# Performance work log

Measured on AMD Instinct MI355X. Metric: run time of the kernel, lower is better.

Reference implementation:

```python
import jax, jax.numpy as jnp
import numpy as np

N = 4194304   # variable nodes
M = 2097152   # check nodes
DC = 10       # max check degree


def setup_inputs() -> dict:
    key = jax.random.key(0)
    k1, k2 = jax.random.split(key)
    cn_adj = jax.random.randint(k1, (M, DC), 0, N, dtype=jnp.int32)
    # pad: last neighbor slot of every other check is empty (-1)
    cn_adj = cn_adj.at[:, -1].set(jnp.where(jnp.arange(M) % 2 == 0, -1, cn_adj[:, -1]))
    llr0 = jax.random.normal(k2, (N,), jnp.float32)
    gamma = jnp.ones((), jnp.float32)  # learnable scaling (learn_gamma=True)
    return {"llr0": llr0, "gamma": gamma, "cn_adj": cn_adj, "n_iter": 5}


def _bp(llr0, gamma, cn_adj, n_iter):
    n = llr0.shape[0]
    valid = cn_adj >= 0
    # original gathers v2c[cn_adj] with raw -1 entries -> numpy-style wrap to index n-1
    gather_idx = jnp.where(valid, cn_adj, n - 1)
    # original masks padded slots out of the scatter-add only
    scatter_idx = jnp.where(valid, cn_adj, 0)

    def bp_step(v2c, _):
        msgs = v2c[gather_idx]                               # (M, DC) gather
        sign = jnp.prod(jnp.sign(msgs + 1e-12), axis=1)      # (M,)
        mag = jnp.min(jnp.abs(msgs), axis=1)                 # (M,) min-sum magnitude
        c2v = gamma * sign * mag                             # (M,) scaled min-sum
        msg = jnp.where(valid, c2v[:, None], 0.0)            # mask padded edges
        v_sum = jnp.zeros(n, llr0.dtype).at[scatter_idx].add(msg)  # scatter-add to variables
        return llr0 + v_sum - v2c, None

    v2c0 = jnp.zeros(n, llr0.dtype)
    v2c_final, _ = jax.lax.scan(bp_step, v2c0, None, length=n_iter)
    return llr0 + v2c_final


def reference(llr0, gamma, cn_adj, n_iter):
    return _bp(llr0, gamma, cn_adj, n_iter)
```

## Files before the change

### kernel.cpp

```cpp
#include <hip/hip_runtime.h>
#include <hip/hip_fp16.h>

#define DCC 10
#define NB 2048
#define NBLK 256
#define HTHREADS 1024

typedef int iv4 __attribute__((ext_vector_type(4)));


__global__ __launch_bounds__(256) void bp_init2_kernel(
    const float* __restrict__ llr0, float* __restrict__ v2c,
    unsigned short* __restrict__ v2c_h, int Nq) {
  int i = blockIdx.x * blockDim.x + threadIdx.x;
  if (i >= Nq) return;
  float4 l = reinterpret_cast<const float4*>(llr0)[i];
  reinterpret_cast<float4*>(v2c)[i] = l;
  reinterpret_cast<__half2*>(v2c_h)[2 * i]     = __floats2half2_rn(l.x, l.y);
  reinterpret_cast<__half2*>(v2c_h)[2 * i + 1] = __floats2half2_rn(l.z, l.w);
}

__global__ __launch_bounds__(HTHREADS) void bp_hist_kernel(
    const int* __restrict__ adj, unsigned* __restrict__ hist,
    int i4_per_block, int i4_total) {
  __shared__ unsigned h[NB];
  for (int i = threadIdx.x; i < NB; i += HTHREADS) h[i] = 0u;
  __syncthreads();
  const iv4* p = reinterpret_cast<const iv4*>(adj);
  int base = blockIdx.x * i4_per_block;
  int lim = base + i4_per_block;
  if (lim > i4_total) lim = i4_total;
  for (int g = base + (int)threadIdx.x; g < lim; g += HTHREADS) {
    iv4 r = __builtin_nontemporal_load(p + g);
    if (r.x >= 0) atomicAdd(&h[(unsigned)r.x >> 11], 1u);
    if (r.y >= 0) atomicAdd(&h[(unsigned)r.y >> 11], 1u);
    if (r.z >= 0) atomicAdd(&h[(unsigned)r.z >> 11], 1u);
    if (r.w >= 0) atomicAdd(&h[(unsigned)r.w >> 11], 1u);
  }
  __syncthreads();
  for (int i = threadIdx.x; i < NB; i += HTHREADS)
    hist[(size_t)i * NBLK + blockIdx.x] = h[i];
}

__global__ __launch_bounds__(256) void bp_scan1_kernel(
    unsigned* __restrict__ data, unsigned* __restrict__ sums) {
  __shared__ unsigned ts[256];
  const int base = blockIdx.x * 1024;
  uint4 d = reinterpret_cast<const uint4*>(data + base)[threadIdx.x];
  unsigned tsum = d.x + d.y + d.z + d.w;
  ts[threadIdx.x] = tsum;
  __syncthreads();
  for (int off = 1; off < 256; off <<= 1) {
    unsigned add = ((int)threadIdx.x >= off) ? ts[threadIdx.x - off] : 0u;
    __syncthreads();
    ts[threadIdx.x] += add;
    __syncthreads();
  }
  unsigned run = ts[threadIdx.x] - tsum;
  if (threadIdx.x == 255) sums[blockIdx.x] = ts[255];
  uint4 o;
  o.x = run; run += d.x;
  o.y = run; run += d.y;
  o.z = run; run += d.z;
  o.w = run;
  reinterpret_cast<uint4*>(data + base)[threadIdx.x] = o;
}

__global__ __launch_bounds__(256) void bp_scan2_kernel(
    unsigned* __restrict__ sums, unsigned* __restrict__ total_p, int n) {
  __shared__ unsigned ts[256];
  __shared__ unsigned carry_s;
  if (threadIdx.x == 0) carry_s = 0u;
  __syncthreads();
  for (int c = 0; c < n; c += 256) {
    int idx = c + (int)threadIdx.x;
    unsigned orig = (idx < n) ? sums[idx] : 0u;
    ts[threadIdx.x] = orig;
    __syncthreads();
    for (int off = 1; off < 256; off <<= 1) {
      unsigned add = ((int)threadIdx.x >= off) ? ts[threadIdx.x - off] : 0u;
      __syncthreads();
      ts[threadIdx.x] += add;
      __syncthreads();
    }
    unsigned excl = ts[threadIdx.x] - orig + carry_s;
    if (idx < n) sums[idx] = excl;
    __syncthreads();
    if (threadIdx.x == 0) carry_s += ts[255];
    __syncthreads();
  }
  if (threadIdx.x == 0) *total_p = carry_s;
}

__global__ __launch_bounds__(HTHREADS) void bp_sortscatter_kernel(
    const int* __restrict__ adj, const unsigned* __restrict__ hist_s,
    const unsigned* __restrict__ sums_s, unsigned* __restrict__ recs,
    int i4_per_block, int i4_total) {
  __shared__ unsigned cur[NB];
  for (int i = threadIdx.x; i < NB; i += HTHREADS) {
    unsigned idx = (unsigned)i * NBLK + blockIdx.x;
    cur[i] = hist_s[idx] + sums_s[idx >> 10];
  }
  __syncthreads();
  const iv4* p = reinterpret_cast<const iv4*>(adj);
  int base = blockIdx.x * i4_per_block;
  int lim = base + i4_per_block;
  if (lim > i4_total) lim = i4_total;
  for (int g = base + (int)threadIdx.x; g < lim; g += HTHREADS) {
    iv4 r = __builtin_nontemporal_load(p + g);
    int s4 = g * 4;
    int av[4] = {r.x, r.y, r.z, r.w};
#pragma unroll
    for (int j = 0; j < 4; ++j) {
      int ai = av[j];
      if (ai >= 0) {
        unsigned check = (unsigned)(s4 + j) / DCC;
        unsigned pos = atomicAdd(&cur[(unsigned)ai >> 11], 1u);
        recs[pos] = ((unsigned)(ai & (NB - 1)) << 21) | check;
      }
    }
  }
}

__global__ __launch_bounds__(256) void bp_gather1_kernel(
    const int* __restrict__ adj, const unsigned short* __restrict__ v2c_h,
    unsigned* __restrict__ state, int Mhalf, int N, int lo, int hi) {
  int t = blockIdx.x * blockDim.x + threadIdx.x;
  if (t >= Mhalf) return;
  const iv4* p = reinterpret_cast<const iv4*>(adj + (size_t)t * 2 * DCC);
  iv4 r0 = __builtin_nontemporal_load(p);
  iv4 r1 = __builtin_nontemporal_load(p + 1);
  iv4 r2 = __builtin_nontemporal_load(p + 2);
  iv4 r3 = __builtin_nontemporal_load(p + 3);
  iv4 r4 = __builtin_nontemporal_load(p + 4);
  int a[20] = {r0.x, r0.y, r0.z, r0.w, r1.x, r1.y, r1.z, r1.w,
               r2.x, r2.y, r2.z, r2.w, r3.x, r3.y, r3.z, r3.w,
               r4.x, r4.y, r4.z, r4.w};
  unsigned s2[2];
#pragma unroll
  for (int c = 0; c < 2; ++c) {
    unsigned sgn = 0u;
    unsigned mab = 0x7c00u;
#pragma unroll
    for (int j = 0; j < DCC; ++j) {
      int ai = a[c * DCC + j];
      int gi = (ai >= 0) ? ai : (N - 1);
      if (gi >= lo && gi < hi) {
        unsigned hb = (unsigned)v2c_h[gi];
        unsigned ab = hb & 0x7fffu;
        sgn ^= (ab != 0u) ? (hb & 0x8000u) : 0u;
        mab = (ab < mab) ? ab : mab;
      }
    }
    s2[c] = mab | sgn;
  }
  state[t] = s2[0] | (s2[1] << 16);
}

__global__ __launch_bounds__(256) void bp_gather2_kernel(
    const int* __restrict__ adj, const unsigned short* __restrict__ v2c_h,
    const unsigned* __restrict__ state0, unsigned short* __restrict__ c2v_h,
    const float* __restrict__ gamma_p, int Mhalf, int N, int lo, int hi) {
  int t = blockIdx.x * blockDim.x + threadIdx.x;
  if (t >= Mhalf) return;
  const float gamma = *gamma_p;
  const iv4* p = reinterpret_cast<const iv4*>(adj + (size_t)t * 2 * DCC);
  iv4 r0 = __builtin_nontemporal_load(p);
  iv4 r1 = __builtin_nontemporal_load(p + 1);
  iv4 r2 = __builtin_nontemporal_load(p + 2);
  iv4 r3 = __builtin_nontemporal_load(p + 3);
  iv4 r4 = __builtin_nontemporal_load(p + 4);
  int a[20] = {r0.x, r0.y, r0.z, r0.w, r1.x, r1.y, r1.z, r1.w,
               r2.x, r2.y, r2.z, r2.w, r3.x, r3.y, r3.z, r3.w,
               r4.x, r4.y, r4.z, r4.w};
  unsigned p0 = state0[t];
  unsigned outw = 0u;
#pragma unroll
  for (int c = 0; c < 2; ++c) {
    unsigned sgn = 0u;
    unsigned mab = 0x7c00u;
#pragma unroll
    for (int j = 0; j < DCC; ++j) {
      int ai = a[c * DCC + j];
      int gi = (ai >= 0) ? ai : (N - 1);
      if (gi >= lo && gi < hi) {
        unsigned hb = (unsigned)v2c_h[gi];
        unsigned ab = hb & 0x7fffu;
        sgn ^= (ab != 0u) ? (hb & 0x8000u) : 0u;
        mab = (ab < mab) ? ab : mab;
      }
    }
    unsigned q0 = (c == 0) ? (p0 & 0xffffu) : (p0 >> 16);
    unsigned a0 = q0 & 0x7fffu;
    unsigned ab = (a0 < mab) ? a0 : mab;
    unsigned sg = ((q0 ^ sgn) & 0x8000u);
    float val = gamma * __half2float(__ushort_as_half((unsigned short)ab));
    val = __uint_as_float(__float_as_uint(val) ^ (sg << 16));
    outw |= ((unsigned)__half_as_ushort(__float2half_rn(val))) << (16 * c);
  }
  reinterpret_cast<unsigned*>(c2v_h)[t] = outw;
}

__global__ __launch_bounds__(256) void bp_accvar_kernel(
    const unsigned* __restrict__ recs, const unsigned short* __restrict__ c2v_h,
    const unsigned* __restrict__ hist_s, const unsigned* __restrict__ sums_s,
    const unsigned* __restrict__ total_p, const float* __restrict__ llr0,
    float* __restrict__ v2c, unsigned short* __restrict__ v2c_h,
    float* __restrict__ out) {
  __shared__ __align__(16) float acc[NB];
  const int b = blockIdx.x;
  for (int i = threadIdx.x; i < NB; i += 256) acc[i] = 0.0f;
  unsigned i0 = (unsigned)b * NBLK;
  unsigned start = hist_s[i0] + sums_s[i0 >> 10];
  unsigned end = (b == NB - 1)
                     ? *total_p
                     : (hist_s[i0 + NBLK] + sums_s[(i0 + NBLK) >> 10]);
  __syncthreads();
  for (unsigned e = start + threadIdx.x; e < end; e += 256) {
    unsigned rec = recs[e];
    float val = __half2float(__ushort_as_half(c2v_h[rec & 0x1FFFFFu]));
    atomicAdd(&acc[rec >> 21], val);
  }
  __syncthreads();
  const int gq = b * (NB / 4);
#pragma unroll
  for (int k = 0; k < 2; ++k) {
    int li = k * 256 + (int)threadIdx.x;
    int gi = gq + li;
    float4 l = reinterpret_cast<const float4*>(llr0)[gi];
    float4 v = reinterpret_cast<float4*>(v2c)[gi];
    float4 s = reinterpret_cast<const float4*>(acc)[li];
    float4 nv;
    nv.x = l.x + s.x - v.x;
    nv.y = l.y + s.y - v.y;
    nv.z = l.z + s.z - v.z;
    nv.w = l.w + s.w - v.w;
    reinterpret_cast<float4*>(v2c)[gi] = nv;
    reinterpret_cast<__half2*>(v2c_h)[2 * gi]     = __floats2half2_rn(nv.x, nv.y);
    reinterpret_cast<__half2*>(v2c_h)[2 * gi + 1] = __floats2half2_rn(nv.z, nv.w);
    if (out != nullptr) {
      float4 o;
      o.x = l.x + nv.x;
      o.y = l.y + nv.y;
      o.z = l.z + nv.z;
      o.w = l.w + nv.w;
      reinterpret_cast<float4*>(out)[gi] = o;
    }
  }
}


__global__ __launch_bounds__(256) void bp_init_kernel(
    const float* __restrict__ llr0, float* __restrict__ v2c,
    float* __restrict__ vsum, __half* __restrict__ v2c_h, int Nq) {
  int i = blockIdx.x * blockDim.x + threadIdx.x;
  if (i >= Nq) return;
  float4 l = reinterpret_cast<const float4*>(llr0)[i];
  reinterpret_cast<float4*>(v2c)[i] = l;
  reinterpret_cast<float4*>(vsum)[i] = make_float4(0.f, 0.f, 0.f, 0.f);
  reinterpret_cast<__half2*>(v2c_h)[2 * i]     = __floats2half2_rn(l.x, l.y);
  reinterpret_cast<__half2*>(v2c_h)[2 * i + 1] = __floats2half2_rn(l.z, l.w);
}

__global__ __launch_bounds__(256) void bp_check_kernel(
    const int* __restrict__ adj, const __half* __restrict__ v2c_h,
    float* __restrict__ vsum, const float* __restrict__ gamma_p,
    int Mhalf, int N) {
  int t = blockIdx.x * blockDim.x + threadIdx.x;
  if (t >= Mhalf) return;
  const float gamma = *gamma_p;
  const int4* p = reinterpret_cast<const int4*>(adj + (size_t)t * 2 * DCC);
  int4 r0 = p[0], r1 = p[1], r2 = p[2], r3 = p[3], r4 = p[4];
  int a[20] = {r0.x, r0.y, r0.z, r0.w, r1.x, r1.y, r1.z, r1.w,
               r2.x, r2.y, r2.z, r2.w, r3.x, r3.y, r3.z, r3.w,
               r4.x, r4.y, r4.z, r4.w};
#pragma unroll
  for (int c = 0; c < 2; ++c) {
    unsigned sgnbits = 0u;
    float mag = 3.402823466e+38f;
#pragma unroll
    for (int j = 0; j < DCC; ++j) {
      int ai = a[c * DCC + j];
      int gi = (ai >= 0) ? ai : (N - 1);
      float v = __half2float(v2c_h[gi]);
      sgnbits ^= (__float_as_uint(v + 1e-12f) & 0x80000000u);
      mag = fminf(mag, fabsf(v));
    }
    float c2v = __uint_as_float(__float_as_uint(gamma * mag) ^ sgnbits);
#pragma unroll
    for (int j = 0; j < DCC; ++j) {
      int ai = a[c * DCC + j];
      if (ai >= 0) unsafeAtomicAdd(&vsum[ai], c2v);
    }
  }
}

__global__ __launch_bounds__(256) void bp_var_kernel(
    const float* __restrict__ llr0, float* __restrict__ v2c,
    float* __restrict__ vsum, __half* __restrict__ v2c_h,
    float* __restrict__ out, int Nq) {
  int i = blockIdx.x * blockDim.x + threadIdx.x;
  if (i >= Nq) return;
  float4 l = reinterpret_cast<const float4*>(llr0)[i];
  float4 v = reinterpret_cast<float4*>(v2c)[i];
  float4 s = reinterpret_cast<float4*>(vsum)[i];
  float4 nv;
  nv.x = l.x + s.x - v.x;
  nv.y = l.y + s.y - v.y;
  nv.z = l.z + s.z - v.z;
  nv.w = l.w + s.w - v.w;
  reinterpret_cast<float4*>(v2c)[i] = nv;
  reinterpret_cast<float4*>(vsum)[i] = make_float4(0.f, 0.f, 0.f, 0.f);
  reinterpret_cast<__half2*>(v2c_h)[2 * i]     = __floats2half2_rn(nv.x, nv.y);
  reinterpret_cast<__half2*>(v2c_h)[2 * i + 1] = __floats2half2_rn(nv.z, nv.w);
  if (out != nullptr) {
    float4 o;
    o.x = l.x + nv.x;
    o.y = l.y + nv.y;
    o.z = l.z + nv.z;
    o.w = l.w + nv.w;
    reinterpret_cast<float4*>(out)[i] = o;
  }
}


extern "C" void kernel_launch(void* const* d_in, const int* in_sizes, int n_in,
                              void* d_out, int out_size, void* d_ws, size_t ws_size,
                              hipStream_t stream) {
  const float* llr0  = (const float*)d_in[0];
  const float* gamma = (const float*)d_in[1];
  const int*   adj   = (const int*)d_in[2];
  const int N = in_sizes[0];
  const int M = in_sizes[2] / DCC;
  const int Mh = M / 2;
  const int NITER = 5;
  const int Nq = N / 4;
  const int varBlocks = (Nq + 255) / 256;
  const int chkBlocks = (Mh + 255) / 256;
  const int Nh = N / 2;

  char* w = (char*)d_ws;
  auto carve = [&](size_t bytes) {
    char* r = w;
    w += (bytes + 255) & ~(size_t)255;
    return r;
  };
  float*          v2c    = (float*)carve((size_t)N * 4);
  unsigned short* v2c_h  = (unsigned short*)carve((size_t)N * 2);
  unsigned*       state0 = (unsigned*)carve((size_t)Mh * 4);
  unsigned short* c2v_h  = (unsigned short*)carve((size_t)M * 2);
  unsigned*       hist   = (unsigned*)carve((size_t)NB * NBLK * 4);
  unsigned*       sums   = (unsigned*)carve((size_t)513 * 4);
  unsigned*       recs   = (unsigned*)carve((size_t)M * DCC * 4);
  unsigned*       total_p = sums + 512;
  size_t need = (size_t)(w - (char*)d_ws);

  const int i4_total = (M * DCC) / 4;
  const int i4_per_block = (i4_total + NBLK - 1) / NBLK;

  bool fast = (need <= ws_size) && (N == NB * 2048) && (M <= (1 << 21)) &&
              ((M * DCC) % 4 == 0);

  if (fast) {
    bp_init2_kernel<<<varBlocks, 256, 0, stream>>>(llr0, v2c, v2c_h, Nq);
    bp_hist_kernel<<<NBLK, HTHREADS, 0, stream>>>(adj, hist, i4_per_block, i4_total);
    bp_scan1_kernel<<<(NB * NBLK) / 1024, 256, 0, stream>>>(hist, sums);
    bp_scan2_kernel<<<1, 256, 0, stream>>>(sums, total_p, (NB * NBLK) / 1024);
    bp_sortscatter_kernel<<<NBLK, HTHREADS, 0, stream>>>(adj, hist, sums, recs,
                                                         i4_per_block, i4_total);
    for (int it = 1; it < NITER; ++it) {
      bp_gather1_kernel<<<chkBlocks, 256, 0, stream>>>(
          adj, v2c_h, state0, Mh, N, 0, Nh);
      bp_gather2_kernel<<<chkBlocks, 256, 0, stream>>>(
          adj, v2c_h, state0, c2v_h, gamma, Mh, N, Nh, N);
      float* outp = (it == NITER - 1) ? (float*)d_out : nullptr;
      bp_accvar_kernel<<<NB, 256, 0, stream>>>(
          recs, c2v_h, hist, sums, total_p, llr0, v2c, v2c_h, outp);
    }
  } else {
    float*  fv2c   = (float*)d_ws;
    float*  fvsum  = fv2c + N;
    __half* fv2c_h = (__half*)(fvsum + N);
    bp_init_kernel<<<varBlocks, 256, 0, stream>>>(llr0, fv2c, fvsum, fv2c_h, Nq);
    for (int it = 1; it < NITER; ++it) {
      bp_check_kernel<<<chkBlocks, 256, 0, stream>>>(adj, fv2c_h, fvsum, gamma, Mh, N);
      float* outp = (it == NITER - 1) ? (float*)d_out : nullptr;
      bp_var_kernel<<<varBlocks, 256, 0, stream>>>(llr0, fv2c, fvsum, fv2c_h, outp, Nq);
    }
  }
}
```

Measured before the change: 1.547 ms.

## Fuse split-range gather kernels into one pass and trim final-iteration stores

Replaces the two gather kernels, which each covered half of the variable index range to keep the fp16 v2c table cache-resident, with a single kernel that gathers all neighbors at once. This drops the intermediate state buffer and the second read of the adjacency array. The final iteration now writes only the output, skipping the v2c and v2c_h updates. The histogram block count is also halved, which changes the sort and scan granularity. The cost is that random gathers now span the full 8 MB half table instead of a 4 MB slice, so more of them may miss in cache.

```diff
diff --git a/kernel.cpp b/kernel.cpp
--- a/kernel.cpp
+++ b/kernel.cpp
@@ -3,7 +3,7 @@
 
 #define DCC 10
 #define NB 2048
-#define NBLK 256
+#define NBLK 128
 #define HTHREADS 1024
 
 typedef int iv4 __attribute__((ext_vector_type(4)));
@@ -122,45 +122,10 @@
   }
 }
 
-__global__ __launch_bounds__(256) void bp_gather1_kernel(
+__global__ __launch_bounds__(256) void bp_gatherf_kernel(
     const int* __restrict__ adj, const unsigned short* __restrict__ v2c_h,
-    unsigned* __restrict__ state, int Mhalf, int N, int lo, int hi) {
-  int t = blockIdx.x * blockDim.x + threadIdx.x;
-  if (t >= Mhalf) return;
-  const iv4* p = reinterpret_cast<const iv4*>(adj + (size_t)t * 2 * DCC);
-  iv4 r0 = __builtin_nontemporal_load(p);
-  iv4 r1 = __builtin_nontemporal_load(p + 1);
-  iv4 r2 = __builtin_nontemporal_load(p + 2);
-  iv4 r3 = __builtin_nontemporal_load(p + 3);
-  iv4 r4 = __builtin_nontemporal_load(p + 4);
-  int a[20] = {r0.x, r0.y, r0.z, r0.w, r1.x, r1.y, r1.z, r1.w,
-               r2.x, r2.y, r2.z, r2.w, r3.x, r3.y, r3.z, r3.w,
-               r4.x, r4.y, r4.z, r4.w};
-  unsigned s2[2];
-#pragma unroll
-  for (int c = 0; c < 2; ++c) {
-    unsigned sgn = 0u;
-    unsigned mab = 0x7c00u;
-#pragma unroll
-    for (int j = 0; j < DCC; ++j) {
-      int ai = a[c * DCC + j];
-      int gi = (ai >= 0) ? ai : (N - 1);
-      if (gi >= lo && gi < hi) {
-        unsigned hb = (unsigned)v2c_h[gi];
-        unsigned ab = hb & 0x7fffu;
-        sgn ^= (ab != 0u) ? (hb & 0x8000u) : 0u;
-        mab = (ab < mab) ? ab : mab;
-      }
-    }
-    s2[c] = mab | sgn;
-  }
-  state[t] = s2[0] | (s2[1] << 16);
-}
-
-__global__ __launch_bounds__(256) void bp_gather2_kernel(
-    const int* __restrict__ adj, const unsigned short* __restrict__ v2c_h,
-    const unsigned* __restrict__ state0, unsigned short* __restrict__ c2v_h,
-    const float* __restrict__ gamma_p, int Mhalf, int N, int lo, int hi) {
+    unsigned short* __restrict__ c2v_h, const float* __restrict__ gamma_p,
+    int Mhalf, int N) {
   int t = blockIdx.x * blockDim.x + threadIdx.x;
   if (t >= Mhalf) return;
   const float gamma = *gamma_p;
@@ -173,7 +138,6 @@
   int a[20] = {r0.x, r0.y, r0.z, r0.w, r1.x, r1.y, r1.z, r1.w,
                r2.x, r2.y, r2.z, r2.w, r3.x, r3.y, r3.z, r3.w,
                r4.x, r4.y, r4.z, r4.w};
-  unsigned p0 = state0[t];
   unsigned outw = 0u;
 #pragma unroll
   for (int c = 0; c < 2; ++c) {
@@ -183,19 +147,13 @@
     for (int j = 0; j < DCC; ++j) {
       int ai = a[c * DCC + j];
       int gi = (ai >= 0) ? ai : (N - 1);
-      if (gi >= lo && gi < hi) {
-        unsigned hb = (unsigned)v2c_h[gi];
-        unsigned ab = hb & 0x7fffu;
-        sgn ^= (ab != 0u) ? (hb & 0x8000u) : 0u;
-        mab = (ab < mab) ? ab : mab;
-      }
-    }
-    unsigned q0 = (c == 0) ? (p0 & 0xffffu) : (p0 >> 16);
-    unsigned a0 = q0 & 0x7fffu;
-    unsigned ab = (a0 < mab) ? a0 : mab;
-    unsigned sg = ((q0 ^ sgn) & 0x8000u);
-    float val = gamma * __half2float(__ushort_as_half((unsigned short)ab));
-    val = __uint_as_float(__float_as_uint(val) ^ (sg << 16));
+      unsigned hb = (unsigned)v2c_h[gi];
+      unsigned ab = hb & 0x7fffu;
+      sgn ^= (ab != 0u) ? (hb & 0x8000u) : 0u;
+      mab = (ab < mab) ? ab : mab;
+    }
+    float val = gamma * __half2float(__ushort_as_half((unsigned short)mab));
+    val = __uint_as_float(__float_as_uint(val) ^ (sgn << 16));
     outw |= ((unsigned)__half_as_ushort(__float2half_rn(val))) << (16 * c);
   }
   reinterpret_cast<unsigned*>(c2v_h)[t] = outw;
@@ -235,9 +193,6 @@
     nv.y = l.y + s.y - v.y;
     nv.z = l.z + s.z - v.z;
     nv.w = l.w + s.w - v.w;
-    reinterpret_cast<float4*>(v2c)[gi] = nv;
-    reinterpret_cast<__half2*>(v2c_h)[2 * gi]     = __floats2half2_rn(nv.x, nv.y);
-    reinterpret_cast<__half2*>(v2c_h)[2 * gi + 1] = __floats2half2_rn(nv.z, nv.w);
     if (out != nullptr) {
       float4 o;
       o.x = l.x + nv.x;
@@ -245,6 +200,10 @@
       o.z = l.z + nv.z;
       o.w = l.w + nv.w;
       reinterpret_cast<float4*>(out)[gi] = o;
+    } else {
+      reinterpret_cast<float4*>(v2c)[gi] = nv;
+      reinterpret_cast<__half2*>(v2c_h)[2 * gi]     = __floats2half2_rn(nv.x, nv.y);
+      reinterpret_cast<__half2*>(v2c_h)[2 * gi + 1] = __floats2half2_rn(nv.z, nv.w);
     }
   }
 }
@@ -337,7 +296,6 @@
   const int Nq = N / 4;
   const int varBlocks = (Nq + 255) / 256;
   const int chkBlocks = (Mh + 255) / 256;
-  const int Nh = N / 2;
 
   char* w = (char*)d_ws;
   auto carve = [&](size_t bytes) {
@@ -347,7 +305,6 @@
   };
   float*          v2c    = (float*)carve((size_t)N * 4);
   unsigned short* v2c_h  = (unsigned short*)carve((size_t)N * 2);
-  unsigned*       state0 = (unsigned*)carve((size_t)Mh * 4);
   unsigned short* c2v_h  = (unsigned short*)carve((size_t)M * 2);
   unsigned*       hist   = (unsigned*)carve((size_t)NB * NBLK * 4);
   unsigned*       sums   = (unsigned*)carve((size_t)513 * 4);
@@ -357,6 +314,7 @@
 
   const int i4_total = (M * DCC) / 4;
   const int i4_per_block = (i4_total + NBLK - 1) / NBLK;
+  const int scanN = (NB * NBLK) / 1024;
 
   bool fast = (need <= ws_size) && (N == NB * 2048) && (M <= (1 << 21)) &&
               ((M * DCC) % 4 == 0);
@@ -364,15 +322,13 @@
   if (fast) {
     bp_init2_kernel<<<varBlocks, 256, 0, stream>>>(llr0, v2c, v2c_h, Nq);
     bp_hist_kernel<<<NBLK, HTHREADS, 0, stream>>>(adj, hist, i4_per_block, i4_total);
-    bp_scan1_kernel<<<(NB * NBLK) / 1024, 256, 0, stream>>>(hist, sums);
-    bp_scan2_kernel<<<1, 256, 0, stream>>>(sums, total_p, (NB * NBLK) / 1024);
+    bp_scan1_kernel<<<scanN, 256, 0, stream>>>(hist, sums);
+    bp_scan2_kernel<<<1, 256, 0, stream>>>(sums, total_p, scanN);
     bp_sortscatter_kernel<<<NBLK, HTHREADS, 0, stream>>>(adj, hist, sums, recs,
                                                          i4_per_block, i4_total);
     for (int it = 1; it < NITER; ++it) {
-      bp_gather1_kernel<<<chkBlocks, 256, 0, stream>>>(
-          adj, v2c_h, state0, Mh, N, 0, Nh);
-      bp_gather2_kernel<<<chkBlocks, 256, 0, stream>>>(
-          adj, v2c_h, state0, c2v_h, gamma, Mh, N, Nh, N);
+      bp_gatherf_kernel<<<chkBlocks, 256, 0, stream>>>(
+          adj, v2c_h, c2v_h, gamma, Mh, N);
       float* outp = (it == NITER - 1) ? (float*)d_out : nullptr;
       bp_accvar_kernel<<<NB, 256, 0, stream>>>(
           recs, c2v_h, hist, sums, total_p, llr0, v2c, v2c_h, outp);
```

Result: slower. 1.793 ms (+15.9%).

## Buffer sort-scatter records in LDS and flush per-bin chunks of eight

Applied to the files above, without the earlier changes.

The counting-sort scatter now stages records per bin in an 8-entry shared-memory ring and flushes each full group of eight as contiguous global writes, instead of issuing one random 4-byte global store per edge. This is meant to improve write coalescing in the one-time edge bucketing pass, at the cost of 80 KB+ of LDS per block, two extra barriers per phase, and lower occupancy. Separately, the last iteration's accumulate kernel skips writing v2c and v2c_h, since only the output is needed after it.

```diff
diff --git a/kernel.cpp b/kernel.cpp
--- a/kernel.cpp
+++ b/kernel.cpp
@@ -96,29 +96,57 @@
     const int* __restrict__ adj, const unsigned* __restrict__ hist_s,
     const unsigned* __restrict__ sums_s, unsigned* __restrict__ recs,
     int i4_per_block, int i4_total) {
-  __shared__ unsigned cur[NB];
+  __shared__ unsigned gstart[NB];
+  __shared__ unsigned cnt[NB];
+  __shared__ unsigned flushed[NB];
+  __shared__ unsigned buf[NB * 8];
   for (int i = threadIdx.x; i < NB; i += HTHREADS) {
     unsigned idx = (unsigned)i * NBLK + blockIdx.x;
-    cur[i] = hist_s[idx] + sums_s[idx >> 10];
+    gstart[i] = hist_s[idx] + sums_s[idx >> 10];
+    cnt[i] = 0u;
+    flushed[i] = 0u;
   }
   __syncthreads();
   const iv4* p = reinterpret_cast<const iv4*>(adj);
   int base = blockIdx.x * i4_per_block;
   int lim = base + i4_per_block;
   if (lim > i4_total) lim = i4_total;
-  for (int g = base + (int)threadIdx.x; g < lim; g += HTHREADS) {
-    iv4 r = __builtin_nontemporal_load(p + g);
-    int s4 = g * 4;
-    int av[4] = {r.x, r.y, r.z, r.w};
-#pragma unroll
-    for (int j = 0; j < 4; ++j) {
-      int ai = av[j];
-      if (ai >= 0) {
-        unsigned check = (unsigned)(s4 + j) / DCC;
-        unsigned pos = atomicAdd(&cur[(unsigned)ai >> 11], 1u);
-        recs[pos] = ((unsigned)(ai & (NB - 1)) << 21) | check;
+  for (int ph = base; ph < lim; ph += HTHREADS) {
+    int g = ph + (int)threadIdx.x;
+    if (g < lim) {
+      iv4 r = __builtin_nontemporal_load(p + g);
+      int s4 = g * 4;
+      int av[4] = {r.x, r.y, r.z, r.w};
+#pragma unroll
+      for (int j = 0; j < 4; ++j) {
+        int ai = av[j];
+        if (ai >= 0) {
+          unsigned bin = (unsigned)ai >> 11;
+          unsigned rec =
+              ((unsigned)(ai & (NB - 1)) << 21) | ((unsigned)(s4 + j) / DCC);
+          unsigned pos = atomicAdd(&cnt[bin], 1u);
+          if (pos < flushed[bin] + 8u)
+            buf[bin * 8 + (pos & 7u)] = rec;
+          else
+            recs[gstart[bin] + pos] = rec;
+        }
       }
     }
+    __syncthreads();
+    for (int b = threadIdx.x; b < NB; b += HTHREADS) {
+      unsigned c = cnt[b], f = flushed[b];
+      if (c - f >= 8u) {
+        unsigned gp = gstart[b] + f;
+#pragma unroll
+        for (int k = 0; k < 8; ++k) recs[gp + k] = buf[b * 8 + ((f + k) & 7u)];
+        flushed[b] = c;
+      }
+    }
+    __syncthreads();
+  }
+  for (int b = threadIdx.x; b < NB; b += HTHREADS) {
+    unsigned c = cnt[b], f = flushed[b], gp = gstart[b];
+    for (unsigned q = f; q < c; ++q) recs[gp + q] = buf[b * 8 + (q & 7u)];
   }
 }
 
@@ -235,9 +263,6 @@
     nv.y = l.y + s.y - v.y;
     nv.z = l.z + s.z - v.z;
     nv.w = l.w + s.w - v.w;
-    reinterpret_cast<float4*>(v2c)[gi] = nv;
-    reinterpret_cast<__half2*>(v2c_h)[2 * gi]     = __floats2half2_rn(nv.x, nv.y);
-    reinterpret_cast<__half2*>(v2c_h)[2 * gi + 1] = __floats2half2_rn(nv.z, nv.w);
     if (out != nullptr) {
       float4 o;
       o.x = l.x + nv.x;
@@ -245,6 +270,10 @@
       o.z = l.z + nv.z;
       o.w = l.w + nv.w;
       reinterpret_cast<float4*>(out)[gi] = o;
+    } else {
+      reinterpret_cast<float4*>(v2c)[gi] = nv;
+      reinterpret_cast<__half2*>(v2c_h)[2 * gi]     = __floats2half2_rn(nv.x, nv.y);
+      reinterpret_cast<__half2*>(v2c_h)[2 * gi + 1] = __floats2half2_rn(nv.z, nv.w);
     }
   }
 }
@@ -357,6 +386,7 @@
 
   const int i4_total = (M * DCC) / 4;
   const int i4_per_block = (i4_total + NBLK - 1) / NBLK;
+  const int scanN = (NB * NBLK) / 1024;
 
   bool fast = (need <= ws_size) && (N == NB * 2048) && (M <= (1 << 21)) &&
               ((M * DCC) % 4 == 0);
@@ -364,8 +394,8 @@
   if (fast) {
     bp_init2_kernel<<<varBlocks, 256, 0, stream>>>(llr0, v2c, v2c_h, Nq);
     bp_hist_kernel<<<NBLK, HTHREADS, 0, stream>>>(adj, hist, i4_per_block, i4_total);
-    bp_scan1_kernel<<<(NB * NBLK) / 1024, 256, 0, stream>>>(hist, sums);
-    bp_scan2_kernel<<<1, 256, 0, stream>>>(sums, total_p, (NB * NBLK) / 1024);
+    bp_scan1_kernel<<<scanN, 256, 0, stream>>>(hist, sums);
+    bp_scan2_kernel<<<1, 256, 0, stream>>>(sums, total_p, scanN);
     bp_sortscatter_kernel<<<NBLK, HTHREADS, 0, stream>>>(adj, hist, sums, recs,
                                                          i4_per_block, i4_total);
     for (int it = 1; it < NITER; ++it) {
```

New measurement: 1.337 ms. 1.16x faster.
